# Kernel tuning notes

Hardware: AMD Instinct MI355X
Metric: run time of the kernel (lower is better)

Reference implementation:

```python
import jax, jax.numpy as jnp
import numpy as np

BETA_MAX = 0.01
CD_WEIGHT = 1.0
FIDELITY_WEIGHT = 0.5
BETA = BETA_MAX  # fully annealed (step >= beta_warmup)
EPS = 1e-12


def _pairwise_dist(a, b):
    """Euclidean distance matrix. a: [B,N,3], b: [B,M,3] -> [B,N,M]."""
    a2 = jnp.sum(a * a, axis=-1)                      # [B,N]
    b2 = jnp.sum(b * b, axis=-1)                      # [B,M]
    ab = jnp.einsum('bnd,bmd->bnm', a, b)             # [B,N,M]
    sq = a2[:, :, None] + b2[:, None, :] - 2.0 * ab
    return jnp.sqrt(jnp.maximum(sq, EPS))


def chamfer_distance_l1(pred, full):
    d = _pairwise_dist(pred, full)                    # [B,N,M]
    d_pf = jnp.min(d, axis=2)                         # pred -> full, [B,N]
    d_fp = jnp.min(d, axis=1)                         # full -> pred, [B,M]
    return 0.5 * (jnp.mean(d_pf) + jnp.mean(d_fp))


def fidelity_loss(partial, pred):
    # one-directional: every partial point should have a close predicted point
    d = _pairwise_dist(partial, pred)                 # [B,P,N]
    return jnp.mean(jnp.min(d, axis=2))


def kl_divergence(mu, logvar):
    # -0.5 * E_batch[ sum_dim (1 + logvar - mu^2 - exp(logvar)) ]
    kl = -0.5 * jnp.sum(1.0 + logvar - mu * mu - jnp.exp(logvar), axis=1)
    return jnp.mean(kl)


def setup_inputs() -> dict:
    key = jax.random.key(0)
    k1, k2, k3, k4, k5 = jax.random.split(key, 5)
    B, N, P, D = 8, 8192, 2048, 512
    return {
        'pred': jax.random.normal(k1, (B, N, 3), dtype=jnp.float32),
        'full': jax.random.normal(k2, (B, N, 3), dtype=jnp.float32),
        'partial': jax.random.normal(k3, (B, P, 3), dtype=jnp.float32),
        'mu': jax.random.normal(k4, (B, D), dtype=jnp.float32),
        'logvar': jax.random.normal(k5, (B, D), dtype=jnp.float32) * 0.1,
    }


def reference(pred, full, partial, mu, logvar):
    cd = chamfer_distance_l1(pred, full)
    kl = kl_divergence(mu, logvar)
    fidel = fidelity_loss(partial, pred)
    total = CD_WEIGHT * cd + BETA * kl + FIDELITY_WEIGHT * fidel
    return (total, cd, kl, fidel)
```

## Files before the change

kernel.cpp:

```cpp
#include <hip/hip_runtime.h>
#include <math.h>

#define BATCH 8
#define NPTS  8192
#define PPTS  2048
#define DLAT  512

typedef __attribute__((ext_vector_type(8)))  short short8;
typedef __attribute__((ext_vector_type(16))) float floatx16;

#define SEG      (2 * BATCH * NPTS + BATCH * PPTS)
#define DIR_PF   0
#define DIR_FP   (BATCH * NPTS)
#define DIR_FID  (2 * BATCH * NPTS)
#define OFF_ACC  (2 * SEG)
#define OFF_CNT  (OFF_ACC + 4)

#define YSPLIT 2
#define YHALF  (NPTS / YSPLIT)
#define CHUNK  512

__device__ __forceinline__ unsigned short f2bf(float f) {
    unsigned int u = __float_as_uint(f);
    return (unsigned short)((u + 0x7FFFu + ((u >> 16) & 1u)) >> 16);
}
__device__ __forceinline__ float bf2f(unsigned short s) {
    return __uint_as_float(((unsigned int)s) << 16);
}

__device__ __forceinline__ float min16(floatx16 d, float prev) {
    float a0 = fminf(fminf(d[0],  d[1]),  d[2]);
    float a1 = fminf(fminf(d[3],  d[4]),  d[5]);
    float a2 = fminf(fminf(d[6],  d[7]),  d[8]);
    float a3 = fminf(fminf(d[9],  d[10]), d[11]);
    float a4 = fminf(fminf(d[12], d[13]), d[14]);
    float b0 = fminf(fminf(a0, a1), a2);
    float b1 = fminf(fminf(a3, a4), d[15]);
    return fminf(fminf(b0, b1), prev);
}

__global__ void init_acc_kernel(unsigned int* __restrict__ ws) {
    const int t = threadIdx.x;
    if (t < 4) ((float*)(ws + OFF_ACC))[t] = 0.0f;
    if (t == 4) ws[OFF_CNT] = 0u;
}

__global__ __launch_bounds__(256) void minpass_kernel(
        const float* __restrict__ pred,
        const float* __restrict__ full,
        const float* __restrict__ partial,
        float* __restrict__ wsf) {
    const int bid = blockIdx.x;
    const int ys  = bid & 1;
    const int r   = bid >> 1;
    const int b   = r / 72;
    const int s   = r % 72;

    const float* xset; const float* yset; int minoff;
    int xbase;
    if (s < 32)      { xset = pred;    yset = full; xbase = b*NPTS + s*256;
                       minoff = ys*SEG + DIR_PF  + b*NPTS + s*256; }
    else if (s < 64) { xset = full;    yset = pred; xbase = b*NPTS + (s-32)*256;
                       minoff = ys*SEG + DIR_FP  + b*NPTS + (s-32)*256; }
    else             { xset = partial; yset = pred; xbase = b*PPTS + (s-64)*256;
                       minoff = ys*SEG + DIR_FID + b*PPTS + (s-64)*256; }

    const int t    = threadIdx.x;
    const int lane = t & 63;
    const int wid  = t >> 6;
    const int l31  = lane & 31;
    const int half = lane >> 5;

    __shared__ uint4 sY[2][CHUNK];
    __shared__ uint4 sX[2][256];
    __shared__ float sXn[256];

    {
        const float* xp = xset + (size_t)(xbase + t) * 3;
        const float x0 = xp[0], x1 = xp[1], x2 = xp[2];
        const float m0 = -2.0f*x0, m1 = -2.0f*x1, m2 = -2.0f*x2;
        const unsigned short h0 = f2bf(m0), h1 = f2bf(m1), h2 = f2bf(m2);
        const unsigned short l0 = f2bf(m0 - bf2f(h0));
        const unsigned short l1 = f2bf(m1 - bf2f(h1));
        const unsigned short l2 = f2bf(m2 - bf2f(h2));
        const unsigned int one = 0x3F80u;
        uint4 r0, r1;
        r0.x = (unsigned int)h0 | ((unsigned int)h1 << 16);
        r0.y = (unsigned int)h2 | ((unsigned int)h0 << 16);
        r0.z = (unsigned int)h1 | ((unsigned int)h2 << 16);
        r0.w = (unsigned int)l0 | ((unsigned int)l1 << 16);
        r1.x = (unsigned int)l2 | (one << 16);
        r1.y = one;
        r1.z = 0u; r1.w = 0u;
        sX[0][t] = r0; sX[1][t] = r1;
        sXn[t] = fmaf(x0, x0, fmaf(x1, x1, x2 * x2));
    }
    __syncthreads();

    const short8 bf0 = *(const short8*)&sX[half][wid*64 + l31];
    const short8 bf1 = *(const short8*)&sX[half][wid*64 + 32 + l31];
    const float  xn0 = sXn[wid*64 + l31];
    const float  xn1 = sXn[wid*64 + 32 + l31];

    const floatx16 zc = {0,0,0,0, 0,0,0,0, 0,0,0,0, 0,0,0,0};
    float cmin0 = 3.4e38f, cmin1 = 3.4e38f;

    const float* ypts = yset + (size_t)(b * NPTS + ys * YHALF) * 3;

    for (int c = 0; c < YHALF; c += CHUNK) {
        __syncthreads();
        for (int i = t; i < CHUNK; i += 256) {
            const float* yp = ypts + (size_t)(c + i) * 3;
            const float y0 = yp[0], y1 = yp[1], y2 = yp[2];
            const unsigned short h0 = f2bf(y0), h1 = f2bf(y1), h2 = f2bf(y2);
            const unsigned short l0 = f2bf(y0 - bf2f(h0));
            const unsigned short l1 = f2bf(y1 - bf2f(h1));
            const unsigned short l2 = f2bf(y2 - bf2f(h2));
            const float yn = fmaf(y0, y0, fmaf(y1, y1, y2 * y2));
            const unsigned short nh = f2bf(yn);
            const unsigned short nl = f2bf(yn - bf2f(nh));
            uint4 r0, r1;
            r0.x = (unsigned int)h0 | ((unsigned int)h1 << 16);
            r0.y = (unsigned int)h2 | ((unsigned int)l0 << 16);
            r0.z = (unsigned int)l1 | ((unsigned int)l2 << 16);
            r0.w = (unsigned int)h0 | ((unsigned int)h1 << 16);
            r1.x = (unsigned int)h2 | ((unsigned int)nh << 16);
            r1.y = (unsigned int)nl;
            r1.z = 0u; r1.w = 0u;
            sY[0][i] = r0; sY[1][i] = r1;
        }
        __syncthreads();

        for (int j = 0; j < CHUNK / 32; ++j) {
            const short8 af = *(const short8*)&sY[half][j * 32 + l31];
            const floatx16 d0 = __builtin_amdgcn_mfma_f32_32x32x16_bf16(af, bf0, zc, 0, 0, 0);
            const floatx16 d1 = __builtin_amdgcn_mfma_f32_32x32x16_bf16(af, bf1, zc, 0, 0, 0);
            cmin0 = min16(d0, cmin0);
            cmin1 = min16(d1, cmin1);
        }
    }

    const float m0 = fminf(cmin0, __shfl_xor(cmin0, 32, 64));
    const float m1 = fminf(cmin1, __shfl_xor(cmin1, 32, 64));
    if (lane < 32) {
        wsf[minoff + wid*64 + l31]      = fmaxf(m0 + xn0, 0.0f);
        wsf[minoff + wid*64 + 32 + l31] = fmaxf(m1 + xn1, 0.0f);
    }
}

__device__ __forceinline__ float waveReduceSum(float v) {
#pragma unroll
    for (int o = 32; o > 0; o >>= 1) v += __shfl_down(v, o, 64);
    return v;
}

__device__ __forceinline__ float blockReduceSum(float v) {
    __shared__ float wsum[4];
    const int lane = threadIdx.x & 63;
    const int wid  = threadIdx.x >> 6;
    v = waveReduceSum(v);
    if (lane == 0) wsum[wid] = v;
    __syncthreads();
    if (wid == 0) {
        v = (lane < ((int)blockDim.x >> 6)) ? wsum[lane] : 0.0f;
        v = waveReduceSum(v);
    }
    return v;
}

#define NRED_BLOCKS 145
__global__ __launch_bounds__(256) void reduce_finalize_kernel(
        float* __restrict__ wsf,
        const float* __restrict__ mu,
        const float* __restrict__ logvar,
        float* __restrict__ out) {
    float* acc = wsf + OFF_ACC;
    unsigned int* cnt = (unsigned int*)wsf + OFF_CNT;
    const int bid = blockIdx.x;
    const int t   = threadIdx.x;

    float v = 0.0f;
    int accIdx;
    if (bid < 144) {
        int base;
        if (bid < 64)       { accIdx = 0; base = DIR_PF  + bid * 1024;         }
        else if (bid < 128) { accIdx = 1; base = DIR_FP  + (bid - 64) * 1024;  }
        else                { accIdx = 2; base = DIR_FID + (bid - 128) * 1024; }
#pragma unroll
        for (int k = 0; k < 4; ++k) {
            const int i = base + k * 256 + t;
            const float m = fminf(wsf[i], wsf[SEG + i]);
            v += sqrtf(fmaxf(m, 1e-12f));
        }
    } else {
        accIdx = 3;
#pragma unroll
        for (int k = 0; k < BATCH * DLAT / 256; ++k) {
            const int i = k * 256 + t;
            const float m = mu[i];
            const float l = logvar[i];
            v += -0.5f * (1.0f + l - m * m - expf(l));
        }
    }

    v = blockReduceSum(v);
    if (t == 0) {
        atomicAdd(&acc[accIdx], v);
        __threadfence();
        const unsigned int done = atomicAdd(cnt, 1u);
        if (done == NRED_BLOCKS - 1) {
            const float s_pf  = atomicAdd(&acc[0], 0.0f);
            const float s_fp  = atomicAdd(&acc[1], 0.0f);
            const float s_fid = atomicAdd(&acc[2], 0.0f);
            const float s_kl  = atomicAdd(&acc[3], 0.0f);
            const float cd  = 0.5f * (s_pf / (float)(BATCH * NPTS) +
                                      s_fp / (float)(BATCH * NPTS));
            const float fid = s_fid / (float)(BATCH * PPTS);
            const float kl  = s_kl / (float)BATCH;
            out[0] = cd + 0.01f * kl + 0.5f * fid;
            out[1] = cd;
            out[2] = kl;
            out[3] = fid;
        }
    }
}

extern "C" void kernel_launch(void* const* d_in, const int* in_sizes, int n_in,
                              void* d_out, int out_size, void* d_ws, size_t ws_size,
                              hipStream_t stream) {
    const float* pred    = (const float*)d_in[0];
    const float* full    = (const float*)d_in[1];
    const float* partial = (const float*)d_in[2];
    const float* mu      = (const float*)d_in[3];
    const float* logvar  = (const float*)d_in[4];
    float* out = (float*)d_out;

    float* wsf = (float*)d_ws;

    init_acc_kernel<<<1, 64, 0, stream>>>((unsigned int*)d_ws);

    minpass_kernel<<<8 * 72 * YSPLIT, 256, 0, stream>>>(pred, full, partial, wsf);

    reduce_finalize_kernel<<<NRED_BLOCKS, 256, 0, stream>>>(wsf, mu, logvar, out);
}
```

Measured before the change: 127.4 us.

## Split Y range four ways, fold accumulator init into minpass, prefetch LDS operands

The Y point range is now split across up to four blocks per X tile, chosen at runtime from workspace size, which raises the grid from 1152 to 2304 blocks to fill more CUs. The separate init kernel is removed and block 0 of the minpass kernel zeroes the accumulators instead. Y staging loads two points per thread with float2 loads, and the MFMA loop is unrolled with a software prefetch of the next LDS operand. The cost is a larger workspace and more partial-min traffic in the reduce kernel. Zeroing from block 0 is safe only because the reduce kernel runs after minpass finishes.

```diff
diff --git a/kernel.cpp b/kernel.cpp
--- a/kernel.cpp
+++ b/kernel.cpp
@@ -13,12 +13,9 @@
 #define DIR_PF   0
 #define DIR_FP   (BATCH * NPTS)
 #define DIR_FID  (2 * BATCH * NPTS)
-#define OFF_ACC  (2 * SEG)
-#define OFF_CNT  (OFF_ACC + 4)
-
-#define YSPLIT 2
-#define YHALF  (NPTS / YSPLIT)
-#define CHUNK  512
+#define OFF_SEG  8
+
+#define CHUNK 512
 
 __device__ __forceinline__ unsigned short f2bf(float f) {
     unsigned int u = __float_as_uint(f);
@@ -39,33 +36,52 @@
     return fminf(fminf(b0, b1), prev);
 }
 
-__global__ void init_acc_kernel(unsigned int* __restrict__ ws) {
-    const int t = threadIdx.x;
-    if (t < 4) ((float*)(ws + OFF_ACC))[t] = 0.0f;
-    if (t == 4) ws[OFF_CNT] = 0u;
+__device__ __forceinline__ void encodeY(float y0, float y1, float y2,
+                                        uint4* r0, uint4* r1) {
+    const unsigned short h0 = f2bf(y0), h1 = f2bf(y1), h2 = f2bf(y2);
+    const unsigned short l0 = f2bf(y0 - bf2f(h0));
+    const unsigned short l1 = f2bf(y1 - bf2f(h1));
+    const unsigned short l2 = f2bf(y2 - bf2f(h2));
+    const float yn = fmaf(y0, y0, fmaf(y1, y1, y2 * y2));
+    const unsigned short nh = f2bf(yn);
+    const unsigned short nl = f2bf(yn - bf2f(nh));
+    r0->x = (unsigned int)h0 | ((unsigned int)h1 << 16);
+    r0->y = (unsigned int)h2 | ((unsigned int)l0 << 16);
+    r0->z = (unsigned int)l1 | ((unsigned int)l2 << 16);
+    r0->w = (unsigned int)h0 | ((unsigned int)h1 << 16);
+    r1->x = (unsigned int)h2 | ((unsigned int)nh << 16);
+    r1->y = (unsigned int)nl;
+    r1->z = 0u; r1->w = 0u;
 }
 
 __global__ __launch_bounds__(256) void minpass_kernel(
         const float* __restrict__ pred,
         const float* __restrict__ full,
         const float* __restrict__ partial,
-        float* __restrict__ wsf) {
+        float* __restrict__ wsf,
+        int ysplit) {
     const int bid = blockIdx.x;
-    const int ys  = bid & 1;
-    const int r   = bid >> 1;
+    const int ys  = bid % ysplit;
+    const int r   = bid / ysplit;
     const int b   = r / 72;
     const int s   = r % 72;
-
-    const float* xset; const float* yset; int minoff;
-    int xbase;
+    const int yhalf = NPTS / ysplit;
+
+    const int t = threadIdx.x;
+
+    if (bid == 0) {
+        if (t < 4) wsf[t] = 0.0f;
+        if (t == 4) ((unsigned int*)wsf)[4] = 0u;
+    }
+
+    const float* xset; const float* yset; int minoff; int xbase;
     if (s < 32)      { xset = pred;    yset = full; xbase = b*NPTS + s*256;
-                       minoff = ys*SEG + DIR_PF  + b*NPTS + s*256; }
+                       minoff = OFF_SEG + ys*SEG + DIR_PF  + b*NPTS + s*256; }
     else if (s < 64) { xset = full;    yset = pred; xbase = b*NPTS + (s-32)*256;
-                       minoff = ys*SEG + DIR_FP  + b*NPTS + (s-32)*256; }
+                       minoff = OFF_SEG + ys*SEG + DIR_FP  + b*NPTS + (s-32)*256; }
     else             { xset = partial; yset = pred; xbase = b*PPTS + (s-64)*256;
-                       minoff = ys*SEG + DIR_FID + b*PPTS + (s-64)*256; }
-
-    const int t    = threadIdx.x;
+                       minoff = OFF_SEG + ys*SEG + DIR_FID + b*PPTS + (s-64)*256; }
+
     const int lane = t & 63;
     const int wid  = t >> 6;
     const int l31  = lane & 31;
@@ -105,38 +121,33 @@
     const floatx16 zc = {0,0,0,0, 0,0,0,0, 0,0,0,0, 0,0,0,0};
     float cmin0 = 3.4e38f, cmin1 = 3.4e38f;
 
-    const float* ypts = yset + (size_t)(b * NPTS + ys * YHALF) * 3;
-
-    for (int c = 0; c < YHALF; c += CHUNK) {
+    const float* ypts = yset + (size_t)(b * NPTS + ys * yhalf) * 3;
+
+    for (int c = 0; c < yhalf; c += CHUNK) {
         __syncthreads();
-        for (int i = t; i < CHUNK; i += 256) {
-            const float* yp = ypts + (size_t)(c + i) * 3;
-            const float y0 = yp[0], y1 = yp[1], y2 = yp[2];
-            const unsigned short h0 = f2bf(y0), h1 = f2bf(y1), h2 = f2bf(y2);
-            const unsigned short l0 = f2bf(y0 - bf2f(h0));
-            const unsigned short l1 = f2bf(y1 - bf2f(h1));
-            const unsigned short l2 = f2bf(y2 - bf2f(h2));
-            const float yn = fmaf(y0, y0, fmaf(y1, y1, y2 * y2));
-            const unsigned short nh = f2bf(yn);
-            const unsigned short nl = f2bf(yn - bf2f(nh));
+        {
+            const float2* yp2 = (const float2*)(ypts + (size_t)(c + 2 * t) * 3);
+            const float2 pa = yp2[0], pb = yp2[1], pc = yp2[2];
             uint4 r0, r1;
-            r0.x = (unsigned int)h0 | ((unsigned int)h1 << 16);
-            r0.y = (unsigned int)h2 | ((unsigned int)l0 << 16);
-            r0.z = (unsigned int)l1 | ((unsigned int)l2 << 16);
-            r0.w = (unsigned int)h0 | ((unsigned int)h1 << 16);
-            r1.x = (unsigned int)h2 | ((unsigned int)nh << 16);
-            r1.y = (unsigned int)nl;
-            r1.z = 0u; r1.w = 0u;
-            sY[0][i] = r0; sY[1][i] = r1;
+            encodeY(pa.x, pa.y, pb.x, &r0, &r1);
+            sY[0][2*t]   = r0; sY[1][2*t]   = r1;
+            encodeY(pb.y, pc.x, pc.y, &r0, &r1);
+            sY[0][2*t+1] = r0; sY[1][2*t+1] = r1;
         }
         __syncthreads();
 
+        const uint4* sYh = &sY[half][0];
+        short8 af = *(const short8*)&sYh[l31];
+#pragma unroll
         for (int j = 0; j < CHUNK / 32; ++j) {
-            const short8 af = *(const short8*)&sY[half][j * 32 + l31];
+            short8 afn = af;
+            if (j + 1 < CHUNK / 32)
+                afn = *(const short8*)&sYh[(j + 1) * 32 + l31];
             const floatx16 d0 = __builtin_amdgcn_mfma_f32_32x32x16_bf16(af, bf0, zc, 0, 0, 0);
             const floatx16 d1 = __builtin_amdgcn_mfma_f32_32x32x16_bf16(af, bf1, zc, 0, 0, 0);
             cmin0 = min16(d0, cmin0);
             cmin1 = min16(d1, cmin1);
+            af = afn;
         }
     }
 
@@ -173,9 +184,10 @@
         float* __restrict__ wsf,
         const float* __restrict__ mu,
         const float* __restrict__ logvar,
-        float* __restrict__ out) {
-    float* acc = wsf + OFF_ACC;
-    unsigned int* cnt = (unsigned int*)wsf + OFF_CNT;
+        float* __restrict__ out,
+        int ysplit) {
+    float* acc = wsf;
+    unsigned int* cnt = (unsigned int*)wsf + 4;
     const int bid = blockIdx.x;
     const int t   = threadIdx.x;
 
@@ -188,8 +200,9 @@
         else                { accIdx = 2; base = DIR_FID + (bid - 128) * 1024; }
 #pragma unroll
         for (int k = 0; k < 4; ++k) {
-            const int i = base + k * 256 + t;
-            const float m = fminf(wsf[i], wsf[SEG + i]);
+            const int i = OFF_SEG + base + k * 256 + t;
+            float m = wsf[i];
+            for (int sg = 1; sg < ysplit; ++sg) m = fminf(m, wsf[sg * SEG + i]);
             v += sqrtf(fmaxf(m, 1e-12f));
         }
     } else {
@@ -234,12 +247,12 @@
     const float* mu      = (const float*)d_in[3];
     const float* logvar  = (const float*)d_in[4];
     float* out = (float*)d_out;
-
     float* wsf = (float*)d_ws;
 
-    init_acc_kernel<<<1, 64, 0, stream>>>((unsigned int*)d_ws);
-
-    minpass_kernel<<<8 * 72 * YSPLIT, 256, 0, stream>>>(pred, full, partial, wsf);
-
-    reduce_finalize_kernel<<<NRED_BLOCKS, 256, 0, stream>>>(wsf, mu, logvar, out);
-}
+    const size_t need4 = (size_t)(OFF_SEG + 4 * SEG) * 4;
+    const int ysplit = (ws_size >= need4) ? 4 : 2;
+
+    minpass_kernel<<<8 * 72 * ysplit, 256, 0, stream>>>(pred, full, partial, wsf, ysplit);
+
+    reduce_finalize_kernel<<<NRED_BLOCKS, 256, 0, stream>>>(wsf, mu, logvar, out, ysplit);
+}
```

After: 119.9 us. -5.9%, faster.
